# Performance work log

Hardware: AMD Instinct MI355X
Metric: run time of the kernel (lower is better)

## Reference

```python
import jax, jax.numpy as jnp
import numpy as np

B, S, D = 4, 4096, 64
D_MODEL = 64


def setup_inputs() -> dict:
    key = jax.random.key(0)
    kq, kk, kv, km = jax.random.split(key, 4)
    q = jax.random.normal(kq, (B, S, D), dtype=jnp.float32)
    k = jax.random.normal(kk, (B, S, D), dtype=jnp.float32)
    v = jax.random.normal(kv, (B, S, D), dtype=jnp.float32)
    mask = jax.random.uniform(km, (B, S, S), dtype=jnp.float32)
    return {"q": q, "k": k, "v": v, "mask": mask}


def reference(q, k, v, mask):
    dk = jnp.sqrt(jnp.asarray(D_MODEL, dtype=q.dtype))
    # [B,S,S] scores; multiplicative (non-additive) mask applied pre-softmax
    scaled_qk = jnp.einsum('bqd,bkd->bqk', q, k) / dk
    scaled_qk = scaled_qk * mask
    attn = jax.nn.softmax(scaled_qk, axis=-1)
    return jnp.einsum('bqk,bkd->bqd', attn, v)
```

## Files before the change

kernel.cpp:

```cpp
#include <hip/hip_runtime.h>
#include <hip/hip_bf16.h>

#define S_LEN 4096
#define DH 64
#define NBATCH 4

typedef __attribute__((ext_vector_type(8))) short bf16x8;
typedef __attribute__((ext_vector_type(4))) short bf16x4;
typedef __attribute__((ext_vector_type(4))) float f32x4;

static __device__ __forceinline__ short f2bf(float x) {
  __hip_bfloat16 h = __float2bfloat16(x);
  return *reinterpret_cast<short*>(&h);
}

#define MFMA(a, b, c) __builtin_amdgcn_mfma_f32_16x16x32_bf16((a), (b), (c), 0, 0, 0)

__global__ __launch_bounds__(256) void cvt_q_kernel(const float* __restrict__ q,
                                                    short* __restrict__ qb) {
  int i = (blockIdx.x * 256 + threadIdx.x) * 4;
  f32x4 x = *(const f32x4*)(q + i);
  bf16x4 o;
#pragma unroll
  for (int j = 0; j < 4; ++j) o[j] = f2bf(x[j]);
  *(bf16x4*)(qb + i) = o;
}

__global__ __launch_bounds__(256) void cvt_frag_kernel(const float* __restrict__ k,
                                                       const float* __restrict__ v,
                                                       short* __restrict__ kfrag,
                                                       short* __restrict__ vfrag) {
  __shared__ short kt[32][80];
  __shared__ short vt[32][80];
  const int t = threadIdx.x;
  const int b = blockIdx.x >> 7;
  const int i = blockIdx.x & 127;
  const size_t src0 = ((size_t)b * S_LEN + i * 32) * DH;
  {
    const int row = t >> 3, c0 = (t & 7) * 8;
    const f32x4 xk0 = *(const f32x4*)(k + src0 + row * DH + c0);
    const f32x4 xk1 = *(const f32x4*)(k + src0 + row * DH + c0 + 4);
    const f32x4 xv0 = *(const f32x4*)(v + src0 + row * DH + c0);
    const f32x4 xv1 = *(const f32x4*)(v + src0 + row * DH + c0 + 4);
#pragma unroll
    for (int j = 0; j < 4; ++j) {
      kt[row][c0 + j] = f2bf(xk0[j]);  kt[row][c0 + 4 + j] = f2bf(xk1[j]);
      vt[row][c0 + j] = f2bf(xv0[j]);  vt[row][c0 + 4 + j] = f2bf(xv1[j]);
    }
  }
  __syncthreads();
  const int c = t >> 6, l = t & 63;
  const size_t dst = (((size_t)(b * 128 + i) * 4 + c) * 64 + l) * 8;
  {
    const int kr = ((c >> 1) * 16) + (l & 15);
    const int d0 = ((c & 1) * 32) + (l >> 4) * 8;
    *(bf16x8*)(kfrag + dst) = *(const bf16x8*)&kt[kr][d0];
  }
  {
    bf16x8 f;
    const int col = c * 16 + (l & 15);
    const int r0 = (l >> 4) * 8;
#pragma unroll
    for (int j = 0; j < 8; ++j) f[j] = vt[r0 + j][col];
    *(bf16x8*)(vfrag + dst) = f;
  }
}

__global__ __launch_bounds__(256, 3) void fa_kernel(
    const short* __restrict__ qb, const short* __restrict__ kfrag,
    const short* __restrict__ vfrag, const float* __restrict__ mask,
    float* __restrict__ out) {
  __shared__ __align__(16) short lds_p[4][16][40];
  __shared__ float lds_O[4][16][64];
  __shared__ float lds_l[4][16];

  const int tid = threadIdx.x;
  const int w = tid >> 6;
  const int lane = tid & 63;
  const int quad = lane >> 4;
  const int n16 = lane & 15;
  const int loff = lane * 8;

  const int vb = ((blockIdx.x & 7) << 7) | (blockIdx.x >> 3);
  const int b = vb >> 8;
  const int q0 = (vb & 255) << 4;

  const short* qrow = qb + (size_t)(b * S_LEN + q0 + n16) * DH;
  const bf16x8 aQ0 = *(const bf16x8*)(qrow + quad * 8);
  const bf16x8 aQ1 = *(const bf16x8*)(qrow + 32 + quad * 8);

  f32x4 O0 = {0.f, 0.f, 0.f, 0.f}, O1 = O0, O2 = O0, O3 = O0;
  float lacc = 0.f;

  const float* mrow = mask + ((size_t)b * S_LEN + q0 + n16) * S_LEN + quad * 4;
  const short* kfb = kfrag + (size_t)(b * 128 + w) * 2048;
  const short* vfb = vfrag + (size_t)(b * 128 + w) * 2048;

  bf16x8 kA0, kA1, kA2, kA3, kB0, kB1, kB2, kB3;
  bf16x8 vA0, vA1, vA2, vA3, vB0, vB1, vB2, vB3;
  f32x4 mA0, mA1, mB0, mB1;

#define LOAD_BK(B0, B1, B2, B3, SS)                       \
  {                                                       \
    const short* kf_ = kfb + (size_t)(SS) * 8192 + loff;  \
    B0 = *(const bf16x8*)(kf_);                           \
    B1 = *(const bf16x8*)(kf_ + 512);                     \
    B2 = *(const bf16x8*)(kf_ + 1024);                    \
    B3 = *(const bf16x8*)(kf_ + 1536);                    \
  }

#define LOAD_BV(V0, V1, V2, V3, SS)                       \
  {                                                       \
    const short* vf_ = vfb + (size_t)(SS) * 8192 + loff;  \
    V0 = *(const bf16x8*)(vf_);                           \
    V1 = *(const bf16x8*)(vf_ + 512);                     \
    V2 = *(const bf16x8*)(vf_ + 1024);                    \
    V3 = *(const bf16x8*)(vf_ + 1536);                    \
  }

#define LOAD_MASK(D0, D1, LK)                             \
  {                                                       \
    const float* mp_ = mrow + (LK);                       \
    D0 = *(const f32x4*)(mp_);                            \
    D1 = *(const f32x4*)(mp_ + 16);                       \
  }

#define FA_STEP(K0, K1, K2, K3, V0, V1, V2, V3, M0, M1, SS)                \
  {                                                                        \
    const f32x4 z = {0.f, 0.f, 0.f, 0.f};                                  \
    f32x4 s0 = MFMA(K0, aQ0, z); s0 = MFMA(K1, aQ1, s0);                   \
    f32x4 s1 = MFMA(K2, aQ0, z); s1 = MFMA(K3, aQ1, s1);                   \
    LOAD_BK(K0, K1, K2, K3, ((SS) + 2) & 31);          \
    float p0_[4], p1_[4];                                                  \
    _Pragma("unroll") for (int r = 0; r < 4; ++r) {                        \
      p0_[r] = __expf(s0[r] * 0.125f * M0[r]);                             \
      p1_[r] = __expf(s1[r] * 0.125f * M1[r]);                             \
      lacc += p0_[r] + p1_[r];                                             \
    }                                                                      \
    LOAD_MASK(M0, M1, (((SS) + 2) * 128 + w * 32) & 4095);     \
    bf16x4 w0_, w1_;                                                       \
    _Pragma("unroll") for (int r = 0; r < 4; ++r) {                        \
      w0_[r] = f2bf(p0_[r]); w1_[r] = f2bf(p1_[r]);                        \
    }                                                                      \
    *(bf16x4*)&lds_p[w][n16][quad * 4] = w0_;                              \
    *(bf16x4*)&lds_p[w][n16][16 + quad * 4] = w1_;                         \
    const bf16x8 aP = *(const bf16x8*)&lds_p[w][n16][quad * 8];            \
    O0 = MFMA(aP, V0, O0); O1 = MFMA(aP, V1, O1);                          \
    O2 = MFMA(aP, V2, O2); O3 = MFMA(aP, V3, O3);                          \
    LOAD_BV(V0, V1, V2, V3, ((SS) + 2) & 31);          \
  }

  LOAD_BK(kA0, kA1, kA2, kA3, 0);
  LOAD_BK(kB0, kB1, kB2, kB3, 1);
  LOAD_BV(vA0, vA1, vA2, vA3, 0);
  LOAD_BV(vB0, vB1, vB2, vB3, 1);
  LOAD_MASK(mA0, mA1, w * 32);
  LOAD_MASK(mB0, mB1, 128 + w * 32);

#pragma unroll 1
  for (int it = 0; it < 16; ++it) {
    const int s2 = it * 2;
    FA_STEP(kA0, kA1, kA2, kA3, vA0, vA1, vA2, vA3, mA0, mA1, s2);
    FA_STEP(kB0, kB1, kB2, kB3, vB0, vB1, vB2, vB3, mB0, mB1, s2 + 1);
  }
#undef LOAD_BK
#undef LOAD_BV
#undef LOAD_MASK
#undef FA_STEP

  lacc += __shfl_xor(lacc, 16);
  lacc += __shfl_xor(lacc, 32);

#pragma unroll
  for (int r = 0; r < 4; ++r) {
    const int row = quad * 4 + r;
    lds_O[w][row][n16]      = O0[r];
    lds_O[w][row][16 + n16] = O1[r];
    lds_O[w][row][32 + n16] = O2[r];
    lds_O[w][row][48 + n16] = O3[r];
  }
  if (lane < 16) lds_l[w][lane] = lacc;
  __syncthreads();

  const int r = tid >> 4;
  const int c4 = (tid & 15) << 2;
  const float inv =
      1.0f / (lds_l[0][r] + lds_l[1][r] + lds_l[2][r] + lds_l[3][r]);
  f32x4 acc;
#pragma unroll
  for (int j = 0; j < 4; ++j)
    acc[j] = (lds_O[0][r][c4 + j] + lds_O[1][r][c4 + j] +
              lds_O[2][r][c4 + j] + lds_O[3][r][c4 + j]) * inv;
  *(f32x4*)(out + (size_t)(b * S_LEN + q0 + r) * DH + c4) = acc;
}

extern "C" void kernel_launch(void* const* d_in, const int* in_sizes, int n_in,
                              void* d_out, int out_size, void* d_ws, size_t ws_size,
                              hipStream_t stream) {
  const float* q = (const float*)d_in[0];
  const float* k = (const float*)d_in[1];
  const float* v = (const float*)d_in[2];
  const float* mask = (const float*)d_in[3];
  float* out = (float*)d_out;

  short* qb = (short*)d_ws;
  short* kfrag = qb + (size_t)NBATCH * S_LEN * DH;
  short* vfrag = kfrag + (size_t)NBATCH * S_LEN * DH;

  cvt_q_kernel<<<(NBATCH * S_LEN * DH) / 1024, 256, 0, stream>>>(q, qb);
  cvt_frag_kernel<<<NBATCH * 128, 256, 0, stream>>>(k, v, kfrag, vfrag);
  fa_kernel<<<NBATCH * 256, 256, 0, stream>>>(qb, kfrag, vfrag, mask, out);
}
```

Measured before the change: 405.6 us.

## Split attention blocks into 4 query tiles by 2 key halves

Each block now has 8 waves and covers 64 query rows. The waves form 4 query groups of 16 rows and 2 key partitions of interleaved 32-key chunks, instead of 16 query rows with 4 key partitions. The mask prefetch depth grows to four buffered tiles so more mask loads are in flight, and the epilogue reduces over 2 key partitions. The aim is more K/V reuse across query groups inside a block and better mask latency hiding. The cost is a grid of only 256 large blocks, roughly one per CU, with fewer resident waves than before.

Result: no change. 402.9 us (-0.6%).

```diff
diff --git a/kernel.cpp b/kernel.cpp
--- a/kernel.cpp
+++ b/kernel.cpp
@@ -66,43 +66,46 @@
   }
 }
 
-__global__ __launch_bounds__(256, 3) void fa_kernel(
+__global__ __launch_bounds__(512, 2) void fa_kernel(
     const short* __restrict__ qb, const short* __restrict__ kfrag,
     const short* __restrict__ vfrag, const float* __restrict__ mask,
     float* __restrict__ out) {
-  __shared__ __align__(16) short lds_p[4][16][40];
-  __shared__ float lds_O[4][16][64];
-  __shared__ float lds_l[4][16];
+  __shared__ __align__(16) short lds_p[8][16][40];
+  __shared__ float lds_O[8][16][64];
+  __shared__ float lds_l[8][16];
 
   const int tid = threadIdx.x;
   const int w = tid >> 6;
+  const int wq = w >> 1;
+  const int wk = w & 1;
   const int lane = tid & 63;
   const int quad = lane >> 4;
   const int n16 = lane & 15;
   const int loff = lane * 8;
 
-  const int vb = ((blockIdx.x & 7) << 7) | (blockIdx.x >> 3);
-  const int b = vb >> 8;
-  const int q0 = (vb & 255) << 4;
-
-  const short* qrow = qb + (size_t)(b * S_LEN + q0 + n16) * DH;
+  const int vb = ((blockIdx.x & 7) << 5) | (blockIdx.x >> 3);
+  const int b = vb >> 6;
+  const int q0 = (vb & 63) << 6;
+
+  const int qr = q0 + wq * 16 + n16;
+  const short* qrow = qb + (size_t)(b * S_LEN + qr) * DH;
   const bf16x8 aQ0 = *(const bf16x8*)(qrow + quad * 8);
   const bf16x8 aQ1 = *(const bf16x8*)(qrow + 32 + quad * 8);
 
   f32x4 O0 = {0.f, 0.f, 0.f, 0.f}, O1 = O0, O2 = O0, O3 = O0;
   float lacc = 0.f;
 
-  const float* mrow = mask + ((size_t)b * S_LEN + q0 + n16) * S_LEN + quad * 4;
-  const short* kfb = kfrag + (size_t)(b * 128 + w) * 2048;
-  const short* vfb = vfrag + (size_t)(b * 128 + w) * 2048;
+  const float* mrow = mask + ((size_t)b * S_LEN + qr) * S_LEN + quad * 4;
+  const short* kfb = kfrag + (size_t)(b * 128 + wk) * 2048;
+  const short* vfb = vfrag + (size_t)(b * 128 + wk) * 2048;
 
   bf16x8 kA0, kA1, kA2, kA3, kB0, kB1, kB2, kB3;
   bf16x8 vA0, vA1, vA2, vA3, vB0, vB1, vB2, vB3;
-  f32x4 mA0, mA1, mB0, mB1;
+  f32x4 mA0, mA1, mB0, mB1, mC0, mC1, mD0, mD1;
 
 #define LOAD_BK(B0, B1, B2, B3, SS)                       \
   {                                                       \
-    const short* kf_ = kfb + (size_t)(SS) * 8192 + loff;  \
+    const short* kf_ = kfb + (size_t)(SS) * 4096 + loff;  \
     B0 = *(const bf16x8*)(kf_);                           \
     B1 = *(const bf16x8*)(kf_ + 512);                     \
     B2 = *(const bf16x8*)(kf_ + 1024);                    \
@@ -111,7 +114,7 @@
 
 #define LOAD_BV(V0, V1, V2, V3, SS)                       \
   {                                                       \
-    const short* vf_ = vfb + (size_t)(SS) * 8192 + loff;  \
+    const short* vf_ = vfb + (size_t)(SS) * 4096 + loff;  \
     V0 = *(const bf16x8*)(vf_);                           \
     V1 = *(const bf16x8*)(vf_ + 512);                     \
     V2 = *(const bf16x8*)(vf_ + 1024);                    \
@@ -130,14 +133,14 @@
     const f32x4 z = {0.f, 0.f, 0.f, 0.f};                                  \
     f32x4 s0 = MFMA(K0, aQ0, z); s0 = MFMA(K1, aQ1, s0);                   \
     f32x4 s1 = MFMA(K2, aQ0, z); s1 = MFMA(K3, aQ1, s1);                   \
-    LOAD_BK(K0, K1, K2, K3, ((SS) + 2) & 31);          \
+    LOAD_BK(K0, K1, K2, K3, ((SS) + 2) & 63);          \
     float p0_[4], p1_[4];                                                  \
     _Pragma("unroll") for (int r = 0; r < 4; ++r) {                        \
       p0_[r] = __expf(s0[r] * 0.125f * M0[r]);                             \
       p1_[r] = __expf(s1[r] * 0.125f * M1[r]);                             \
       lacc += p0_[r] + p1_[r];                                             \
     }                                                                      \
-    LOAD_MASK(M0, M1, (((SS) + 2) * 128 + w * 32) & 4095);     \
+    LOAD_MASK(M0, M1, (((SS) + 4) * 64 + wk * 32) & 4095);     \
     bf16x4 w0_, w1_;                                                       \
     _Pragma("unroll") for (int r = 0; r < 4; ++r) {                        \
       w0_[r] = f2bf(p0_[r]); w1_[r] = f2bf(p1_[r]);                        \
@@ -147,21 +150,25 @@
     const bf16x8 aP = *(const bf16x8*)&lds_p[w][n16][quad * 8];            \
     O0 = MFMA(aP, V0, O0); O1 = MFMA(aP, V1, O1);                          \
     O2 = MFMA(aP, V2, O2); O3 = MFMA(aP, V3, O3);                          \
-    LOAD_BV(V0, V1, V2, V3, ((SS) + 2) & 31);          \
+    LOAD_BV(V0, V1, V2, V3, ((SS) + 2) & 63);          \
   }
 
   LOAD_BK(kA0, kA1, kA2, kA3, 0);
   LOAD_BK(kB0, kB1, kB2, kB3, 1);
   LOAD_BV(vA0, vA1, vA2, vA3, 0);
   LOAD_BV(vB0, vB1, vB2, vB3, 1);
-  LOAD_MASK(mA0, mA1, w * 32);
-  LOAD_MASK(mB0, mB1, 128 + w * 32);
+  LOAD_MASK(mA0, mA1, wk * 32);
+  LOAD_MASK(mB0, mB1, 64 + wk * 32);
+  LOAD_MASK(mC0, mC1, 128 + wk * 32);
+  LOAD_MASK(mD0, mD1, 192 + wk * 32);
 
 #pragma unroll 1
   for (int it = 0; it < 16; ++it) {
-    const int s2 = it * 2;
-    FA_STEP(kA0, kA1, kA2, kA3, vA0, vA1, vA2, vA3, mA0, mA1, s2);
-    FA_STEP(kB0, kB1, kB2, kB3, vB0, vB1, vB2, vB3, mB0, mB1, s2 + 1);
+    const int s4 = it * 4;
+    FA_STEP(kA0, kA1, kA2, kA3, vA0, vA1, vA2, vA3, mA0, mA1, s4);
+    FA_STEP(kB0, kB1, kB2, kB3, vB0, vB1, vB2, vB3, mB0, mB1, s4 + 1);
+    FA_STEP(kA0, kA1, kA2, kA3, vA0, vA1, vA2, vA3, mC0, mC1, s4 + 2);
+    FA_STEP(kB0, kB1, kB2, kB3, vB0, vB1, vB2, vB3, mD0, mD1, s4 + 3);
   }
 #undef LOAD_BK
 #undef LOAD_BV
@@ -182,16 +189,20 @@
   if (lane < 16) lds_l[w][lane] = lacc;
   __syncthreads();
 
-  const int r = tid >> 4;
-  const int c4 = (tid & 15) << 2;
-  const float inv =
-      1.0f / (lds_l[0][r] + lds_l[1][r] + lds_l[2][r] + lds_l[3][r]);
-  f32x4 acc;
-#pragma unroll
-  for (int j = 0; j < 4; ++j)
-    acc[j] = (lds_O[0][r][c4 + j] + lds_O[1][r][c4 + j] +
-              lds_O[2][r][c4 + j] + lds_O[3][r][c4 + j]) * inv;
-  *(f32x4*)(out + (size_t)(b * S_LEN + q0 + r) * DH + c4) = acc;
+  const int g = tid >> 7;
+  const int r = (tid >> 3) & 15;
+  const int c8 = (tid & 7) << 3;
+  const int w0 = g * 2, w1 = g * 2 + 1;
+  const float inv = 1.0f / (lds_l[w0][r] + lds_l[w1][r]);
+  float* op = out + (size_t)(b * S_LEN + q0 + g * 16 + r) * DH + c8;
+  f32x4 acc0, acc1;
+#pragma unroll
+  for (int j = 0; j < 4; ++j) {
+    acc0[j] = (lds_O[w0][r][c8 + j]     + lds_O[w1][r][c8 + j])     * inv;
+    acc1[j] = (lds_O[w0][r][c8 + 4 + j] + lds_O[w1][r][c8 + 4 + j]) * inv;
+  }
+  *(f32x4*)(op) = acc0;
+  *(f32x4*)(op + 4) = acc1;
 }
 
 extern "C" void kernel_launch(void* const* d_in, const int* in_sizes, int n_in,
@@ -209,5 +220,5 @@
 
   cvt_q_kernel<<<(NBATCH * S_LEN * DH) / 1024, 256, 0, stream>>>(q, qb);
   cvt_frag_kernel<<<NBATCH * 128, 256, 0, stream>>>(k, v, kfrag, vfrag);
-  fa_kernel<<<NBATCH * 256, 256, 0, stream>>>(qb, kfrag, vfrag, mask, out);
-}
+  fa_kernel<<<NBATCH * 64, 512, 0, stream>>>(qb, kfrag, vfrag, mask, out);
+}
```
